# Performance work log

Hardware: AMD Instinct MI355X
Metric: run time of the kernel (lower is better)

Reference implementation:

```python
import jax, jax.numpy as jnp
import numpy as np

N = 50000
E = 1200000
IN_DIM = 128
HID = 16      # out_channels of conv1 per head
HEADS1 = 8
OUT_DIM = 128  # conv2 out_channels, heads=1
EPS = 1e-16


def _linear_params(key, fan_in, fan_out):
    kw, kb = jax.random.split(key)
    s = 1.0 / np.sqrt(fan_in)
    W = jax.random.uniform(kw, (fan_in, fan_out), minval=-s, maxval=s, dtype=jnp.float32)
    b = jax.random.uniform(kb, (fan_out,), minval=-s, maxval=s, dtype=jnp.float32)
    return W, b


def setup_inputs() -> dict:
    key = jax.random.key(0)
    ks = jax.random.split(key, 10)
    x = jax.random.normal(ks[0], (N, IN_DIM), dtype=jnp.float32)
    edge_index = jax.random.randint(ks[1], (2, E), 0, N, dtype=jnp.int64)
    # conv1: in=128, heads=8, per-head=16 -> H*C = 128
    Wq1, bq1 = _linear_params(ks[2], IN_DIM, HEADS1 * HID)
    Wk1, bk1 = _linear_params(ks[3], IN_DIM, HEADS1 * HID)
    Wv1, bv1 = _linear_params(ks[4], IN_DIM, HEADS1 * HID)
    Ws1, bs1 = _linear_params(ks[5], IN_DIM, HEADS1 * HID)
    # conv2: in=128, heads=1, per-head=OUT_DIM
    Wq2, bq2 = _linear_params(ks[6], HEADS1 * HID, OUT_DIM)
    Wk2, bk2 = _linear_params(ks[7], HEADS1 * HID, OUT_DIM)
    Wv2, bv2 = _linear_params(ks[8], HEADS1 * HID, OUT_DIM)
    Ws2, bs2 = _linear_params(ks[9], HEADS1 * HID, OUT_DIM)
    return dict(x=x, edge_index=edge_index,
                Wq1=Wq1, bq1=bq1, Wk1=Wk1, bk1=bk1, Wv1=Wv1, bv1=bv1, Ws1=Ws1, bs1=bs1,
                Wq2=Wq2, bq2=bq2, Wk2=Wk2, bk2=bk2, Wv2=Wv2, bv2=bv2, Ws2=Ws2, bs2=bs2)


def _transformer_conv(x, src, dst, Wq, bq, Wk, bk, Wv, bv, Ws, bs, heads, ch):
    """PyG TransformerConv (concat=True, root_weight=True, no edge_attr)."""
    n = x.shape[0]
    q = (x @ Wq + bq).reshape(n, heads, ch)
    k = (x @ Wk + bk).reshape(n, heads, ch)
    v = (x @ Wv + bv).reshape(n, heads, ch)
    # per-edge attention logits: message from src j to dst i
    alpha = jnp.einsum('ehc,ehc->eh', q[dst], k[src]) / np.sqrt(ch)  # [E, H]
    # segment softmax over incoming edges of each destination node
    m = jax.ops.segment_max(alpha, dst, num_segments=n)              # [N, H]
    m = jnp.where(jnp.isfinite(m), m, 0.0)
    ea = jnp.exp(alpha - jax.lax.stop_gradient(m)[dst])
    denom = jax.ops.segment_sum(ea, dst, num_segments=n)             # [N, H]
    attn = ea / (denom[dst] + EPS)                                   # [E, H]
    out = jax.ops.segment_sum(attn[:, :, None] * v[src], dst, num_segments=n)  # [N, H, C]
    return out.reshape(n, heads * ch) + (x @ Ws + bs)                # skip (root) connection


def reference(x, edge_index,
              Wq1, bq1, Wk1, bk1, Wv1, bv1, Ws1, bs1,
              Wq2, bq2, Wk2, bk2, Wv2, bv2, Ws2, bs2):
    src, dst = edge_index[0], edge_index[1]
    h = _transformer_conv(x, src, dst, Wq1, bq1, Wk1, bk1, Wv1, bv1, Ws1, bs1, HEADS1, HID)
    out = _transformer_conv(h, src, dst, Wq2, bq2, Wk2, bk2, Wv2, bv2, Ws2, bs2, 1, OUT_DIM)
    return out
```

## Files before the change

### kernel.cpp

```cpp
#include <hip/hip_runtime.h>
#include <cstdint>

#define N_NODES 50000
#define N_EDGES 1200000
#define NP2 50176
#define NSCAN 196
#define BM 64
#define GT 782
#define NWG 1564

typedef __attribute__((ext_vector_type(8))) short short8;
typedef __attribute__((ext_vector_type(4))) float f32x4;

__device__ __forceinline__ unsigned short f2bf(float x) {
    unsigned u = __float_as_uint(x);
    unsigned r = (u + 0x7FFFu + ((u >> 16) & 1u)) >> 16;
    return (unsigned short)r;
}
__device__ __forceinline__ float bf2f(unsigned short h) {
    return __uint_as_float(((unsigned)h) << 16);
}
__device__ __forceinline__ int swz(int row, int kbyte) {
    return row * 256 + (kbyte ^ ((row & 7) << 4));
}

__global__ __launch_bounds__(256) void prep_w(
    const float* __restrict__ W0, const float* __restrict__ W1,
    const float* __restrict__ W2, const float* __restrict__ W3,
    const float* __restrict__ W4, const float* __restrict__ W5,
    const float* __restrict__ W6, const float* __restrict__ W7,
    unsigned short* __restrict__ WTH)
{
    int g = blockIdx.x * 256 + threadIdx.x;
    int m = g >> 14, o = g & 16383;
    int n = o >> 7, k = o & 127;
    const float* W;
    switch (m) {
        case 0: W = W0; break; case 1: W = W1; break;
        case 2: W = W2; break; case 3: W = W3; break;
        case 4: W = W4; break; case 5: W = W5; break;
        case 6: W = W6; break; default: W = W7; break;
    }
    WTH[g] = f2bf(W[k * 128 + n]);
}

__global__ __launch_bounds__(256, 2) void gemm_mfma(
    const float* __restrict__ A, int nrows,
    const unsigned short* __restrict__ WT,
    const float* __restrict__ b0, const float* __restrict__ b1,
    const float* __restrict__ b2, const float* __restrict__ b3,
    float* __restrict__ O0, unsigned short* __restrict__ O1,
    unsigned short* __restrict__ O2, float* __restrict__ O3)
{
    __shared__ unsigned short As[BM * 128];
    __shared__ unsigned short Bs[2 * 128 * 128];

    const int orig = blockIdx.x;
    const int xcd = orig & 7, lid = orig >> 3;
    const int wgid = ((xcd < 4) ? xcd * 196 : 784 + (xcd - 4) * 195) + lid;
    const int xt = wgid >> 1;
    const int p  = wgid & 1;
    const int row0 = xt * BM;
    const int t = threadIdx.x;

    #pragma unroll
    for (int i = 0; i < 4; ++i) {
        int chunk = t + i * 256;
        int row = chunk >> 4, c8 = chunk & 15;
        int gr = row0 + row;
        float4 a0, a1;
        if (gr < nrows) {
            a0 = *(const float4*)(A + (size_t)gr * 128 + c8 * 8);
            a1 = *(const float4*)(A + (size_t)gr * 128 + c8 * 8 + 4);
        } else {
            a0 = make_float4(0.f, 0.f, 0.f, 0.f);
            a1 = a0;
        }
        short8 h;
        h[0] = f2bf(a0.x); h[1] = f2bf(a0.y); h[2] = f2bf(a0.z); h[3] = f2bf(a0.w);
        h[4] = f2bf(a1.x); h[5] = f2bf(a1.y); h[6] = f2bf(a1.z); h[7] = f2bf(a1.w);
        *(short8*)((char*)As + swz(row, c8 * 16)) = h;
    }
    #pragma unroll
    for (int i = 0; i < 16; ++i) {
        int chunk = t + i * 256;
        int o = chunk >> 11, n = (chunk >> 4) & 127, c8 = chunk & 15;
        short8 b = *(const short8*)(WT + ((size_t)(p * 2 + o) * 16384 + n * 128 + c8 * 8));
        *(short8*)((char*)Bs + o * 32768 + swz(n, c8 * 16)) = b;
    }
    __syncthreads();

    const int lane = t & 63;
    const int w    = t >> 6;
    const int o    = w & 1;
    const int rg2  = w >> 1;
    const int mi   = lane & 15;
    const int kg   = lane >> 4;

    f32x4 acc[2][8] = {};

    #pragma unroll
    for (int ks = 0; ks < 4; ++ks) {
        const int kb = ks * 64 + kg * 16;
        short8 a0 = *(const short8*)((char*)As + swz(rg2 * 32 + mi, kb));
        short8 a1 = *(const short8*)((char*)As + swz(rg2 * 32 + 16 + mi, kb));
        #pragma unroll
        for (int ct = 0; ct < 8; ++ct) {
            short8 b = *(const short8*)((char*)Bs + o * 32768 + swz(ct * 16 + mi, kb));
            acc[0][ct] = __builtin_amdgcn_mfma_f32_16x16x32_bf16(a0, b, acc[0][ct], 0, 0, 0);
            acc[1][ct] = __builtin_amdgcn_mfma_f32_16x16x32_bf16(a1, b, acc[1][ct], 0, 0, 0);
        }
    }

    const int out = p * 2 + o;
    const float* bptr = (out == 0) ? b0 : (out == 1) ? b1 : (out == 2) ? b2 : b3;
    const int g2 = lane >> 4;
    #pragma unroll
    for (int ct = 0; ct < 8; ++ct) {
        int col = ct * 16 + mi;
        float bias_v = bptr[col];
        #pragma unroll
        for (int tile = 0; tile < 2; ++tile) {
            #pragma unroll
            for (int r = 0; r < 4; ++r) {
                int grow = row0 + rg2 * 32 + tile * 16 + g2 * 4 + r;
                if (grow < nrows) {
                    float val = acc[tile][ct][r] + bias_v;
                    size_t idx = (size_t)grow * 128 + col;
                    if (out == 0)      O0[idx] = val;
                    else if (out == 1) O1[idx] = f2bf(val);
                    else if (out == 2) O2[idx] = f2bf(val);
                    else               O3[idx] = val;
                }
            }
        }
    }
}

__global__ __launch_bounds__(256) void hist_k(const int* __restrict__ dst, int* __restrict__ deg)
{
    int e = blockIdx.x * 256 + threadIdx.x;
    if (e >= N_EDGES) return;
    atomicAdd(&deg[dst[e]], 1);
}

__global__ __launch_bounds__(256) void scan1_k(const int* __restrict__ deg, int* __restrict__ bsum)
{
    __shared__ int s[256];
    int t = threadIdx.x;
    s[t] = deg[blockIdx.x * 256 + t];
    __syncthreads();
    for (int off = 128; off > 0; off >>= 1) {
        if (t < off) s[t] += s[t + off];
        __syncthreads();
    }
    if (t == 0) bsum[blockIdx.x] = s[0];
}

__global__ __launch_bounds__(256) void scan2_k(const int* __restrict__ bsum, int* __restrict__ boff,
                                               int* __restrict__ rowptr)
{
    __shared__ int s[256];
    int t = threadIdx.x;
    int v = (t < NSCAN) ? bsum[t] : 0;
    s[t] = v;
    __syncthreads();
    for (int off = 1; off < 256; off <<= 1) {
        int v2 = (t >= off) ? s[t - off] : 0;
        __syncthreads();
        s[t] += v2;
        __syncthreads();
    }
    if (t < NSCAN) boff[t] = s[t] - v;
    if (t == 0) rowptr[N_NODES] = N_EDGES;
}

__global__ __launch_bounds__(256) void scan3_k(const int* __restrict__ deg, const int* __restrict__ boff,
                                               int* __restrict__ rowptr, int* __restrict__ cursor)
{
    __shared__ int s[256];
    int t = threadIdx.x;
    int i = blockIdx.x * 256 + t;
    int d = deg[i];
    s[t] = d;
    __syncthreads();
    for (int off = 1; off < 256; off <<= 1) {
        int v2 = (t >= off) ? s[t - off] : 0;
        __syncthreads();
        s[t] += v2;
        __syncthreads();
    }
    if (i < N_NODES) {
        int val = boff[blockIdx.x] + s[t] - d;
        rowptr[i] = val;
        cursor[i] = val;
    }
}

__global__ __launch_bounds__(256) void fill_k(
    const int* __restrict__ src, const int* __restrict__ dst,
    int* __restrict__ cursor, int* __restrict__ esrc)
{
    int e = blockIdx.x * 256 + threadIdx.x;
    if (e >= N_EDGES) return;
    int p = atomicAdd(&cursor[dst[e]], 1);
    esrc[p] = src[e];
}

template<int H>
__global__ __launch_bounds__(256) void fused_attn(
    const float* __restrict__ Qm, const unsigned short* __restrict__ Km,
    const unsigned short* __restrict__ Vm, const float* __restrict__ Sm,
    const int* __restrict__ rowptr, const int* __restrict__ esrc,
    float* __restrict__ out, float scale)
{
    const int n = blockIdx.x * 4 + (threadIdx.x >> 6);
    const int c = threadIdx.x & 63;
    const int start = rowptr[n];
    const int cnt   = rowptr[n + 1] - start;
    float2 q2 = *(const float2*)(Qm + (size_t)n * 128 + 2 * c);
    q2.x *= scale; q2.y *= scale;
    float ax = 0.f, ay = 0.f, den = 0.f;
    for (int base = 0; base < cnt; base += 64) {
        int mm = min(64, cnt - base);
        int my_s = (c < mm) ? esrc[start + base + c] : 0;
        for (int j = 0; j < mm; ++j) {
            int s = __shfl(my_s, j);
            ushort2 kb = *(const ushort2*)(Km + (size_t)s * 128 + 2 * c);
            float p = bf2f(kb.x) * q2.x + bf2f(kb.y) * q2.y;
            if (H == 8) {
                p += __shfl_xor(p, 1);
                p += __shfl_xor(p, 2);
                p += __shfl_xor(p, 4);
            } else {
                #pragma unroll
                for (int o = 1; o < 64; o <<= 1) p += __shfl_xor(p, o);
            }
            float ea = __expf(p);
            ushort2 vb = *(const ushort2*)(Vm + (size_t)s * 128 + 2 * c);
            ax += ea * bf2f(vb.x);
            ay += ea * bf2f(vb.y);
            den += ea;
        }
    }
    float rd = 1.f / (den + 1e-16f);
    float2 s2 = *(const float2*)(Sm + (size_t)n * 128 + 2 * c);
    float2 o2; o2.x = ax * rd + s2.x; o2.y = ay * rd + s2.y;
    *(float2*)(out + (size_t)n * 128 + 2 * c) = o2;
}

extern "C" void kernel_launch(void* const* d_in, const int* in_sizes, int n_in,
                              void* d_out, int out_size, void* d_ws, size_t ws_size,
                              hipStream_t stream)
{
    const float* x       = (const float*)d_in[0];
    const int*   ei      = (const int*)d_in[1];
    const int*   esrc_in = ei;
    const int*   edst_in = ei + N_EDGES;

    const float* Wq1 = (const float*)d_in[2];  const float* bq1 = (const float*)d_in[3];
    const float* Wk1 = (const float*)d_in[4];  const float* bk1 = (const float*)d_in[5];
    const float* Wv1 = (const float*)d_in[6];  const float* bv1 = (const float*)d_in[7];
    const float* Ws1 = (const float*)d_in[8];  const float* bs1 = (const float*)d_in[9];
    const float* Wq2 = (const float*)d_in[10]; const float* bq2 = (const float*)d_in[11];
    const float* Wk2 = (const float*)d_in[12]; const float* bk2 = (const float*)d_in[13];
    const float* Wv2 = (const float*)d_in[14]; const float* bv2 = (const float*)d_in[15];
    const float* Ws2 = (const float*)d_in[16]; const float* bs2 = (const float*)d_in[17];

    float* out = (float*)d_out;

    char* base = (char*)d_ws;
    const size_t NF4 = (size_t)N_NODES * 128 * 4;
    const size_t NF2 = (size_t)N_NODES * 128 * 2;
    size_t off = 0;
    float*          Q    = (float*)(base + off);          off += NF4;
    float*          S    = (float*)(base + off);          off += NF4;
    unsigned short* Kb   = (unsigned short*)(base + off); off += NF2;
    unsigned short* Vb   = (unsigned short*)(base + off); off += NF2;
    unsigned short* WTH  = (unsigned short*)(base + off); off += 8 * 16384 * 2;
    int*            DEG  = (int*)(base + off);            off += (size_t)NP2 * 4;
    int*            ROW  = (int*)(base + off);            off += (size_t)NP2 * 4;
    int*            CUR  = (int*)(base + off);            off += (size_t)NP2 * 4;
    int*            BSUM = (int*)(base + off);            off += 1024;
    int*            BOFF = (int*)(base + off);            off += 1024;
    int*            ESRC = (int*)(base + off);            off += (size_t)N_EDGES * 4;
    if (ws_size < off) return;

    const int EB1 = (N_EDGES + 255) / 256;
    const int FB  = N_NODES / 4;

    hipMemsetAsync(DEG, 0, (size_t)NP2 * 4, stream);

    prep_w<<<512, 256, 0, stream>>>(Wq1, Wk1, Wv1, Ws1, Wq2, Wk2, Wv2, Ws2, WTH);

    hist_k<<<EB1, 256, 0, stream>>>(edst_in, DEG);
    scan1_k<<<NSCAN, 256, 0, stream>>>(DEG, BSUM);
    scan2_k<<<1, 256, 0, stream>>>(BSUM, BOFF, ROW);
    scan3_k<<<NSCAN, 256, 0, stream>>>(DEG, BOFF, ROW, CUR);
    fill_k<<<EB1, 256, 0, stream>>>(esrc_in, edst_in, CUR, ESRC);

    gemm_mfma<<<NWG, 256, 0, stream>>>(x, N_NODES, WTH,
        bq1, bk1, bv1, bs1, Q, Kb, Vb, S);
    fused_attn<8><<<FB, 256, 0, stream>>>(Q, Kb, Vb, S, ROW, ESRC, out, 0.25f);

    gemm_mfma<<<NWG, 256, 0, stream>>>(out, N_NODES, WTH + 4 * 16384,
        bq2, bk2, bv2, bs2, Q, Kb, Vb, S);
    fused_attn<1><<<FB, 256, 0, stream>>>(Q, Kb, Vb, S, ROW, ESRC, out, 0.08838834764831845f);
}
```

Measured before the change: 599.6 us.

## Process eight edges per wavefront concurrently in fused attention kernel

Changes the thread mapping of the fused attention kernel: each wavefront now handles 8 edges at once, and each lane owns a head slice of 16 channels, loading K and V with 16-byte vector loads. This removes the serial per-edge loop and its cross-lane reductions per edge, exposing more memory-level parallelism. In exchange, a cross-lane reduction of 17 values per node is added at the end, register use grows, and lanes sit idle when a node's degree is not a multiple of 8. For the H==1 case the dot product is reduced across 8 lanes.

After: 551.6 us. 1.09x faster.

```diff
diff --git a/kernel.cpp b/kernel.cpp
--- a/kernel.cpp
+++ b/kernel.cpp
@@ -215,38 +215,80 @@
     float* __restrict__ out, float scale)
 {
     const int n = blockIdx.x * 4 + (threadIdx.x >> 6);
-    const int c = threadIdx.x & 63;
+    const int l = threadIdx.x & 63;
+    const int i = l >> 3;
+    const int h = l & 7;
     const int start = rowptr[n];
     const int cnt   = rowptr[n + 1] - start;
-    float2 q2 = *(const float2*)(Qm + (size_t)n * 128 + 2 * c);
-    q2.x *= scale; q2.y *= scale;
-    float ax = 0.f, ay = 0.f, den = 0.f;
-    for (int base = 0; base < cnt; base += 64) {
-        int mm = min(64, cnt - base);
-        int my_s = (c < mm) ? esrc[start + base + c] : 0;
-        for (int j = 0; j < mm; ++j) {
-            int s = __shfl(my_s, j);
-            ushort2 kb = *(const ushort2*)(Km + (size_t)s * 128 + 2 * c);
-            float p = bf2f(kb.x) * q2.x + bf2f(kb.y) * q2.y;
-            if (H == 8) {
-                p += __shfl_xor(p, 1);
-                p += __shfl_xor(p, 2);
-                p += __shfl_xor(p, 4);
-            } else {
-                #pragma unroll
-                for (int o = 1; o < 64; o <<= 1) p += __shfl_xor(p, o);
-            }
-            float ea = __expf(p);
-            ushort2 vb = *(const ushort2*)(Vm + (size_t)s * 128 + 2 * c);
-            ax += ea * bf2f(vb.x);
-            ay += ea * bf2f(vb.y);
-            den += ea;
-        }
-    }
-    float rd = 1.f / (den + 1e-16f);
-    float2 s2 = *(const float2*)(Sm + (size_t)n * 128 + 2 * c);
-    float2 o2; o2.x = ax * rd + s2.x; o2.y = ay * rd + s2.y;
-    *(float2*)(out + (size_t)n * 128 + 2 * c) = o2;
+
+    float q[16];
+    {
+        const float4* qp = (const float4*)(Qm + (size_t)n * 128 + h * 16);
+        #pragma unroll
+        for (int r = 0; r < 4; ++r) {
+            float4 v = qp[r];
+            q[4*r+0] = v.x * scale; q[4*r+1] = v.y * scale;
+            q[4*r+2] = v.z * scale; q[4*r+3] = v.w * scale;
+        }
+    }
+
+    float acc[16];
+    #pragma unroll
+    for (int c = 0; c < 16; ++c) acc[c] = 0.f;
+    float den = 0.f;
+
+    for (int base = 0; base < cnt; base += 8) {
+        const int ei = base + i;
+        const bool valid = ei < cnt;
+        const int s = esrc[start + (valid ? ei : 0)];
+        const short8* kp = (const short8*)(Km + (size_t)s * 128 + h * 16);
+        short8 k0 = kp[0], k1 = kp[1];
+        const short8* vp = (const short8*)(Vm + (size_t)s * 128 + h * 16);
+        short8 v0 = vp[0], v1 = vp[1];
+
+        float d0 = 0.f, d1 = 0.f;
+        #pragma unroll
+        for (int c = 0; c < 8; ++c) {
+            d0 += bf2f((unsigned short)k0[c]) * q[c];
+            d1 += bf2f((unsigned short)k1[c]) * q[8 + c];
+        }
+        float d = d0 + d1;
+        if (H == 1) {
+            d += __shfl_xor(d, 1);
+            d += __shfl_xor(d, 2);
+            d += __shfl_xor(d, 4);
+        }
+        float ea = valid ? __expf(d) : 0.f;
+        den += ea;
+        #pragma unroll
+        for (int c = 0; c < 8; ++c) {
+            acc[c]     += ea * bf2f((unsigned short)v0[c]);
+            acc[8 + c] += ea * bf2f((unsigned short)v1[c]);
+        }
+    }
+
+    #pragma unroll
+    for (int m = 8; m <= 32; m <<= 1) {
+        den += __shfl_xor(den, m);
+        #pragma unroll
+        for (int c = 0; c < 16; ++c) acc[c] += __shfl_xor(acc[c], m);
+    }
+
+    if (l < 8) {
+        float rd = 1.f / (den + 1e-16f);
+        const float4* sp = (const float4*)(Sm + (size_t)n * 128 + l * 16);
+        float4*       op = (float4*)(out + (size_t)n * 128 + l * 16);
+        #pragma unroll
+        for (int r = 0; r < 4; ++r) {
+            float4 sv = sp[r];
+            float4 ov;
+            ov.x = acc[4*r+0] * rd + sv.x;
+            ov.y = acc[4*r+1] * rd + sv.y;
+            ov.z = acc[4*r+2] * rd + sv.z;
+            ov.w = acc[4*r+3] * rd + sv.w;
+            op[r] = ov;
+        }
+    }
 }
 
 extern "C" void kernel_launch(void* const* d_in, const int* in_sizes, int n_in,
```
